# Optimization experiments

Measured on AMD Instinct MI355X. Metric: run time of the kernel, lower is better.

Reference implementation:

```python
import jax, jax.numpy as jnp
import numpy as np

N_DOC, N_WORD = 20000, 80000
N = N_DOC + N_WORD
E = 1_000_000
HID = 64
M = 10000


def setup_inputs() -> dict:
    key = jax.random.key(0)
    ks = jax.random.split(key, 10)
    doc_features = jax.random.normal(ks[0], (N_DOC, 768), dtype=jnp.float32)
    word_features = jax.random.normal(ks[1], (N_WORD, 300), dtype=jnp.float32)
    edge_index = jax.random.randint(ks[2], (2, E), 0, N, dtype=jnp.int64)
    edge_weight = jax.random.uniform(ks[3], (E,), dtype=jnp.float32)
    mask_idx = jax.random.randint(ks[4], (M,), 0, N, dtype=jnp.int64)
    y = jax.random.randint(ks[5], (N,), 0, 4, dtype=jnp.int64)
    s = 0.02
    W_lin = jax.random.normal(ks[6], (300, 768), dtype=jnp.float32) * s
    b_lin = jnp.zeros((768,), dtype=jnp.float32)
    W1 = jax.random.normal(ks[7], (768, HID), dtype=jnp.float32) * s
    b1 = jnp.zeros((HID,), dtype=jnp.float32)
    W2 = jax.random.normal(ks[8], (HID, HID), dtype=jnp.float32) * s
    b2 = jnp.zeros((HID,), dtype=jnp.float32)
    return {"doc_features": doc_features, "word_features": word_features,
            "edge_weight": edge_weight, "W_lin": W_lin, "b_lin": b_lin,
            "W1": W1, "b1": b1, "W2": W2, "b2": b2,
            "edge_index": edge_index, "mask_idx": mask_idx, "y": y}


def _gcn_norm(edge_index, edge_weight, num_nodes):
    # PyG gcn_norm: add self loops (weight 1), symmetric normalization.
    row, col = edge_index[0], edge_index[1]
    loop = jnp.arange(num_nodes, dtype=row.dtype)
    row = jnp.concatenate([row, loop])
    col = jnp.concatenate([col, loop])
    w = jnp.concatenate([edge_weight, jnp.ones((num_nodes,), edge_weight.dtype)])
    deg = jax.ops.segment_sum(w, col, num_segments=num_nodes)
    dis = jnp.where(deg > 0, jax.lax.rsqrt(jnp.maximum(deg, 1e-12)), 0.0)
    norm = dis[row] * w * dis[col]
    return row, col, norm


def _gcn_layer(x, W, b, row, col, norm, num_nodes):
    xw = x @ W                              # [N, out]
    msg = xw[row] * norm[:, None]           # gather + weight  [E+N, out]
    out = jax.ops.segment_sum(msg, col, num_segments=num_nodes)  # scatter-add
    return out + b


def reference(doc_features, word_features, edge_weight, W_lin, b_lin,
              W1, b1, W2, b2, edge_index, mask_idx, y):
    word = word_features @ W_lin + b_lin            # [N_WORD, 768]
    x = jnp.concatenate([doc_features, word], axis=0)  # [N, 768]
    num_nodes = x.shape[0]
    row, col, norm = _gcn_norm(edge_index, edge_weight, num_nodes)
    x = _gcn_layer(x, W1, b1, row, col, norm, num_nodes)
    x = jax.nn.relu(x)
    # dropout is identity in eval mode
    x = _gcn_layer(x, W2, b2, row, col, norm, num_nodes)
    return x[mask_idx], y[mask_idx]
```

## Files before the change

kernel.cpp:

```cpp
#include <hip/hip_runtime.h>


typedef __attribute__((ext_vector_type(8))) short short8;
typedef __attribute__((ext_vector_type(4))) float float4v;

__device__ __forceinline__ unsigned short f2bf(float f) {
  unsigned u = __float_as_uint(f);
  return (unsigned short)((u + 0x7FFFu + ((u >> 16) & 1u)) >> 16);
}
__device__ __forceinline__ float bf2f(unsigned short u) {
  return __uint_as_float((unsigned)u << 16);
}
__device__ __forceinline__ int permcol(int p) {
  return ((p & 3) << 4) | (p >> 2);
}

template <bool PERM>
__device__ __forceinline__ void pack_w_body(const float* __restrict__ W, int K,
                                            int nk0, unsigned short* __restrict__ pack,
                                            int tid) {
  int lane = tid & 63;
  int rest = tid >> 6;
  int k0 = rest % nk0;
  int g = rest / nk0;
  int quad = lane >> 4;
  int n = (lane & 15) + g * 16;
  short8 v;
#pragma unroll
  for (int j = 0; j < 8; ++j) {
    int k = k0 * 32 + quad * 8 + j;
    int ks = PERM ? permcol(k) : k;
    float w = (k < K) ? W[(size_t)ks * 64 + n] : 0.f;
    v[j] = (short)f2bf(w);
  }
  *(short8*)(pack + (((size_t)(g * nk0 + k0) * 64 + lane) << 3)) = v;
}

template <bool LAST, bool BF16PERM, int NK0, int CHUNK>
__device__ __forceinline__ void mfma_gemm_body(
    const float* __restrict__ X, int ldx, const float* __restrict__ lastRow,
    const unsigned short* __restrict__ Wpack,
    int K, const float* __restrict__ bias,
    void* __restrict__ outv, int R, int waveIdx) {
  int r0 = waveIdx * 16;
  if (r0 >= R) return;
  const int lane = threadIdx.x & 63;
  const int quad = lane >> 4;
  const int m = lane & 15;
  const float* xrow = nullptr;
  {
    int row = r0 + m;
    if (row < R) xrow = (LAST && row == R - 1) ? lastRow : X + (size_t)row * ldx;
  }

  float4v acc[4];
#pragma unroll
  for (int g = 0; g < 4; ++g) acc[g] = (float4v){0.f, 0.f, 0.f, 0.f};

#pragma unroll
  for (int c0 = 0; c0 < NK0; c0 += CHUNK) {
    float a[CHUNK][8];
#pragma unroll
    for (int cc = 0; cc < CHUNK; ++cc) {
      int kb = (c0 + cc) * 32 + quad * 8;
      if (xrow && kb + 8 <= K) {
        float4 v0 = *(const float4*)(xrow + kb);
        float4 v1 = *(const float4*)(xrow + kb + 4);
        a[cc][0] = v0.x; a[cc][1] = v0.y; a[cc][2] = v0.z; a[cc][3] = v0.w;
        a[cc][4] = v1.x; a[cc][5] = v1.y; a[cc][6] = v1.z; a[cc][7] = v1.w;
      } else {
#pragma unroll
        for (int j = 0; j < 8; ++j) {
          int k = kb + j;
          a[cc][j] = (xrow && k < K) ? xrow[k] : 0.f;
        }
      }
    }
#pragma unroll
    for (int cc = 0; cc < CHUNK; ++cc) {
      int k0 = c0 + cc;
      short8 bf[4];
#pragma unroll
      for (int g = 0; g < 4; ++g)
        bf[g] = *(const short8*)(Wpack + (((size_t)(g * NK0 + k0) * 64 + lane) << 3));
      short8 af;
#pragma unroll
      for (int j = 0; j < 8; ++j) af[j] = (short)f2bf(a[cc][j]);
#pragma unroll
      for (int g = 0; g < 4; ++g)
        acc[g] = __builtin_amdgcn_mfma_f32_16x16x32_bf16(af, bf[g], acc[g], 0, 0, 0);
    }
  }

  if (BF16PERM) {
    float b0 = bias ? bias[m] : 0.f;
    float b1 = bias ? bias[16 + m] : 0.f;
    float b2 = bias ? bias[32 + m] : 0.f;
    float b3 = bias ? bias[48 + m] : 0.f;
#pragma unroll
    for (int j = 0; j < 4; ++j) {
      int r = r0 + quad * 4 + j;
      if (r < R) {
        ushort4 pk;
        pk.x = f2bf(acc[0][j] + b0);
        pk.y = f2bf(acc[1][j] + b1);
        pk.z = f2bf(acc[2][j] + b2);
        pk.w = f2bf(acc[3][j] + b3);
        *(ushort4*)((unsigned short*)outv + ((size_t)r * 64 + m * 4)) = pk;
      }
    }
  } else {
#pragma unroll
    for (int g = 0; g < 4; ++g) {
      float b = bias ? bias[g * 16 + m] : 0.f;
#pragma unroll
      for (int reg = 0; reg < 4; ++reg) {
        int r = r0 + quad * 4 + reg;
        if (r < R) ((float*)outv)[(size_t)r * 64 + g * 16 + m] = acc[g][reg] + b;
      }
    }
  }
}

__global__ __launch_bounds__(256) void k_pack(
    const float* __restrict__ W1, unsigned short* __restrict__ packW1,
    const float* __restrict__ W2, unsigned short* __restrict__ packW2,
    int* __restrict__ bucketTot, int nbuck) {
  int b = blockIdx.x;
  int t = threadIdx.x;
  if (b < 24) { pack_w_body<false>(W1, 768, 24, packW1, b * 256 + t); return; }
  b -= 24;
  if (b < 2) { pack_w_body<true>(W2, 64, 2, packW2, b * 256 + t); return; }
  for (int i = t; i < nbuck + 2; i += 256) bucketTot[i] = 0;
}

__global__ __launch_bounds__(256) void k_pre(
    const float* __restrict__ Wlin, const float* __restrict__ blin,
    const unsigned short* __restrict__ packW1, float* __restrict__ WfuseB,
    int histBlocks, int fuseBlocks,
    const int* __restrict__ ei, int E, int* __restrict__ bucketTot, int nbuck,
    const float* __restrict__ doc, unsigned short* __restrict__ xw1, int ND) {
  int b = blockIdx.x;
  int t = threadIdx.x;
  if (b < histBlocks) {
    __shared__ int h[512];
    h[t] = 0; h[t + 256] = 0;
    __syncthreads();
    int e0 = b * 4096;
#pragma unroll 4
    for (int i = 0; i < 16; ++i) {
      int e = e0 + t + i * 256;
      if (e < E) atomicAdd(&h[ei[E + e] >> 8], 1);
    }
    __syncthreads();
    if (t < nbuck && h[t]) atomicAdd(bucketTot + t, h[t]);
    if (t + 256 < nbuck && h[t + 256]) atomicAdd(bucketTot + t + 256, h[t + 256]);
    return;
  }
  b -= histBlocks;
  if (b < fuseBlocks) {
    mfma_gemm_body<true, false, 24, 8>(Wlin, 768, blin, packW1, 768,
                                       nullptr, WfuseB, 301, b * 4 + (t >> 6));
    return;
  }
  b -= fuseBlocks;
  mfma_gemm_body<false, true, 24, 8>(doc, 768, nullptr, packW1, 768,
                                     nullptr, xw1, ND, b * 4 + (t >> 6));
}

__global__ __launch_bounds__(512) void k_scanB(
    const int* __restrict__ bucketTot, int nbuck,
    int* __restrict__ bucketBase, int* __restrict__ bucketRun,
    const float* __restrict__ WfuseB, unsigned short* __restrict__ packWf) {
  int t = threadIdx.x;
  if (blockIdx.x > 0) {
    pack_w_body<false>(WfuseB, 300, 10, packWf, ((int)blockIdx.x - 1) * 512 + t);
    return;
  }
  __shared__ int s[512];
  int v = (t < nbuck) ? bucketTot[t] : 0;
  s[t] = v; __syncthreads();
  for (int off = 1; off < 512; off <<= 1) {
    int x = (t >= off) ? s[t - off] : 0;
    __syncthreads();
    s[t] += x;
    __syncthreads();
  }
  if (t < nbuck) {
    int ex = s[t] - v;
    bucketBase[t] = ex;
    bucketRun[t] = ex;
  }
  if (t == nbuck - 1) bucketBase[nbuck] = s[t];
}

__global__ __launch_bounds__(256) void k_sd(
    const int* __restrict__ ei, const float* __restrict__ ew, int E,
    int scatBlocks, int* __restrict__ bucketRun, int2* __restrict__ ebuf,
    const float* __restrict__ wordf, const unsigned short* __restrict__ packWf,
    const float* __restrict__ bfuse, unsigned short* __restrict__ xw1word, int NWsd) {
  int b = blockIdx.x;
  int t = threadIdx.x;
  if (b >= scatBlocks) {
    mfma_gemm_body<false, true, 10, 5>(wordf, 300, nullptr, packWf, 300,
                                       bfuse, xw1word, NWsd, (b - scatBlocks) * 4 + (t >> 6));
    return;
  }
  __shared__ int h[512];
  __shared__ int base[512];
  __shared__ int cur[512];
  h[t] = 0; h[t + 256] = 0;
  __syncthreads();
  int e0 = b * 4096;
#pragma unroll 4
  for (int i = 0; i < 16; ++i) {
    int e = e0 + t + i * 256;
    if (e < E) atomicAdd(&h[ei[E + e] >> 8], 1);
  }
  __syncthreads();
#pragma unroll
  for (int k = t; k < 512; k += 256) {
    if (h[k]) base[k] = atomicAdd(bucketRun + k, h[k]);
    cur[k] = 0;
  }
  __syncthreads();
#pragma unroll 4
  for (int i = 0; i < 16; ++i) {
    int e = e0 + t + i * 256;
    if (e < E) {
      int d = ei[E + e];
      int bk = d >> 8;
      int r = base[bk] + atomicAdd(&cur[bk], 1);
      ebuf[r] = make_int2(ei[e] | ((d & 255) << 17), __float_as_int(ew[e]));
    }
  }
}

__global__ __launch_bounds__(256) void k_bw(
    const int2* __restrict__ ebuf, const int* __restrict__ bucketBase,
    int nbuck, int N, int* __restrict__ offs, float* __restrict__ dis,
    int2* __restrict__ entries,
    const float* __restrict__ wordf2, const unsigned short* __restrict__ packWf,
    const float* __restrict__ bfuse, unsigned short* __restrict__ xw1word2, int NW2) {
  int b = blockIdx.x;
  int t = threadIdx.x;
  if (b >= nbuck) {
    mfma_gemm_body<false, true, 10, 5>(wordf2, 300, nullptr, packWf, 300,
                                       bfuse, xw1word2, NW2, (b - nbuck) * 4 + (t >> 6));
    return;
  }
  __shared__ int scnt[256];
  __shared__ float swd[256];
  __shared__ int sscan[256];
  __shared__ int scur[256];
  int node0 = b << 8;
  int nn = min(256, N - node0);
  int estart = bucketBase[b], eend = bucketBase[b + 1];
  scnt[t] = (t < nn) ? 1 : 0;
  swd[t] = (t < nn) ? 1.f : 0.f;
  __syncthreads();
  for (int p = estart + t; p < eend; p += 256) {
    int2 e = ebuf[p];
    int low = (e.x >> 17) & 255;
    atomicAdd(&scnt[low], 1);
    atomicAdd(&swd[low], __int_as_float(e.y));
  }
  __syncthreads();
  int v = scnt[t];
  sscan[t] = v; __syncthreads();
  for (int off = 1; off < 256; off <<= 1) {
    int x = (t >= off) ? sscan[t - off] : 0;
    __syncthreads();
    sscan[t] += x;
    __syncthreads();
  }
  int excl = sscan[t] - v;
  int entriesBase = estart + node0;
  if (t < nn) {
    offs[node0 + t] = entriesBase + excl;
    dis[node0 + t] = rsqrtf(fmaxf(swd[t], 1e-12f));
    entries[entriesBase + excl] = make_int2(node0 + t, __float_as_int(1.0f));
  }
  scur[t] = excl + 1;
  if (t == 0 && b == nbuck - 1) offs[N] = entriesBase + (eend - estart) + nn;
  __syncthreads();
  for (int p = estart + t; p < eend; p += 256) {
    int2 e = ebuf[p];
    int low = (e.x >> 17) & 255;
    int r = atomicAdd(&scur[low], 1);
    entries[entriesBase + r] = make_int2(e.x & 0x1FFFF, e.y);
  }
}

__device__ __forceinline__ void row_gather2(const unsigned short* __restrict__ xin,
                                            const int2* __restrict__ entries,
                                            const float* __restrict__ dis,
                                            int p, int pe, int l32,
                                            float& ra0, float& ra1) {
  float a0 = 0.f, a1 = 0.f;
  for (; p + 8 <= pe; p += 8) {
    int2 e[8];
#pragma unroll
    for (int j = 0; j < 8; ++j) e[j] = entries[p + j];
    unsigned x[8];
    float ds[8];
#pragma unroll
    for (int j = 0; j < 8; ++j) {
      x[j] = *(const unsigned*)(xin + ((size_t)e[j].x << 6) + (l32 << 1));
      ds[j] = dis[e[j].x];
    }
#pragma unroll
    for (int j = 0; j < 8; ++j) {
      float w = __int_as_float(e[j].y) * ds[j];
      a0 = fmaf(bf2f((unsigned short)(x[j] & 0xffffu)), w, a0);
      a1 = fmaf(bf2f((unsigned short)(x[j] >> 16)), w, a1);
    }
  }
  if (p + 4 <= pe) {
    int2 e[4];
#pragma unroll
    for (int j = 0; j < 4; ++j) e[j] = entries[p + j];
    unsigned x[4];
    float ds[4];
#pragma unroll
    for (int j = 0; j < 4; ++j) {
      x[j] = *(const unsigned*)(xin + ((size_t)e[j].x << 6) + (l32 << 1));
      ds[j] = dis[e[j].x];
    }
#pragma unroll
    for (int j = 0; j < 4; ++j) {
      float w = __int_as_float(e[j].y) * ds[j];
      a0 = fmaf(bf2f((unsigned short)(x[j] & 0xffffu)), w, a0);
      a1 = fmaf(bf2f((unsigned short)(x[j] >> 16)), w, a1);
    }
    p += 4;
  }
  for (; p < pe; ++p) {
    int2 e = entries[p];
    unsigned x = *(const unsigned*)(xin + ((size_t)e.x << 6) + (l32 << 1));
    float w = __int_as_float(e.y) * dis[e.x];
    a0 = fmaf(bf2f((unsigned short)(x & 0xffffu)), w, a0);
    a1 = fmaf(bf2f((unsigned short)(x >> 16)), w, a1);
  }
  ra0 = a0; ra1 = a1;
}

__global__ void k_agg(const unsigned short* __restrict__ xin, const int2* __restrict__ entries,
                      const int* __restrict__ offs, const float* __restrict__ dis,
                      const float* __restrict__ bias, unsigned short* __restrict__ xout, int N) {
  const int tid = threadIdx.x;
  const int l32 = tid & 31;
  int i = blockIdx.x * 8 + (tid >> 5);
  if (i >= N) return;
  float a0, a1;
  row_gather2(xin, entries, dis, offs[i], offs[i + 1], l32, a0, a1);
  float d = dis[i];
  a0 = fmaxf(fmaf(a0, d, bias[permcol(2 * l32)]), 0.f);
  a1 = fmaxf(fmaf(a1, d, bias[permcol(2 * l32 + 1)]), 0.f);
  ushort2 pk;
  pk.x = f2bf(a0);
  pk.y = f2bf(a1);
  *(ushort2*)(xout + ((size_t)i << 6) + (l32 << 1)) = pk;
}

__global__ void k_agg2m(const unsigned short* __restrict__ xin, const int2* __restrict__ entries,
                        const int* __restrict__ offs, const float* __restrict__ dis,
                        const int* __restrict__ mask, const int* __restrict__ y,
                        float* __restrict__ tout, float* __restrict__ outY, int M) {
  const int tid = threadIdx.x;
  const int l32 = tid & 31;
  int o = blockIdx.x * 8 + (tid >> 5);
  if (o >= M) return;
  int i = mask[o];
  float a0, a1;
  row_gather2(xin, entries, dis, offs[i], offs[i + 1], l32, a0, a1);
  float d = dis[i];
  float2 pk;
  pk.x = a0 * d;
  pk.y = a1 * d;
  *(float2*)(tout + ((size_t)o << 6) + (l32 << 1)) = pk;
  if (l32 == 0) outY[o] = (float)y[i];
}

__global__ __launch_bounds__(256) void k_mfma_final(
    const float* __restrict__ X, const unsigned short* __restrict__ packW2,
    const float* __restrict__ b2, float* __restrict__ out, int M) {
  mfma_gemm_body<false, false, 2, 2>(X, 64, nullptr, packW2, 64,
                                     b2, out, M, blockIdx.x * 4 + (threadIdx.x >> 6));
}

extern "C" void kernel_launch(void* const* d_in, const int* in_sizes, int n_in,
                              void* d_out, int out_size, void* d_ws, size_t ws_size,
                              hipStream_t stream) {
  const float* doc   = (const float*)d_in[0];
  const float* wordf = (const float*)d_in[1];
  const float* ew    = (const float*)d_in[2];
  const float* Wlin  = (const float*)d_in[3];
  const float* blin  = (const float*)d_in[4];
  const float* W1    = (const float*)d_in[5];
  const float* b1    = (const float*)d_in[6];
  const float* W2    = (const float*)d_in[7];
  const float* b2    = (const float*)d_in[8];
  const int*   ei    = (const int*)d_in[9];
  const int*   mask  = (const int*)d_in[10];
  const int*   y     = (const int*)d_in[11];

  const int E  = in_sizes[2];
  const int M  = in_sizes[10];
  const int ND = in_sizes[0] / 768;
  const int NW = in_sizes[1] / 300;
  const int N  = ND + NW;
  const int NE = N + E;
  const int nbuck = (N + 255) >> 8;

  char* p = (char*)d_ws;
  auto carve = [&](size_t bytes) -> void* {
    void* q = (void*)p;
    p += (bytes + 255) & ~(size_t)255;
    return q;
  };
  float*          WfuseB = (float*)carve(301 * 64 * 4);
  unsigned short* packW1 = (unsigned short*)carve((size_t)4 * 24 * 64 * 8 * 2);
  unsigned short* packW2 = (unsigned short*)carve((size_t)4 * 2 * 64 * 8 * 2);
  unsigned short* packWf = (unsigned short*)carve((size_t)4 * 10 * 64 * 8 * 2);
  float* dis       = (float*)carve((size_t)N * 4);
  int*   offs      = (int*)carve(((size_t)N + 1) * 4);
  int*   bucketTot = (int*)carve((size_t)(nbuck + 2) * 4);
  int*   bucketBase= (int*)carve((size_t)(nbuck + 2) * 4);
  int*   bucketRun = (int*)carve((size_t)(nbuck + 2) * 4);
  int2*  ebuf      = (int2*)carve((size_t)E * 8);
  int2*  entries   = (int2*)carve((size_t)NE * 8);
  unsigned short* xw1 = (unsigned short*)carve((size_t)N * 64 * 2);
  unsigned short* h1  = (unsigned short*)carve((size_t)N * 64 * 2);
  float* tmask = (float*)carve((size_t)M * 64 * 4);

  k_pack<<<27, 256, 0, stream>>>(W1, packW1, W2, packW2, bucketTot, nbuck);

  const int fuseBlocks = (301 + 63) / 64;
  const int docBlocks  = (ND + 63) / 64;
  const int histBlocks = (E + 4095) / 4096;
  k_pre<<<histBlocks + fuseBlocks + docBlocks, 256, 0, stream>>>(
      Wlin, blin, packW1, WfuseB, histBlocks, fuseBlocks,
      ei, E, bucketTot, nbuck, doc, xw1, ND);

  k_scanB<<<6, 512, 0, stream>>>(bucketTot, nbuck, bucketBase, bucketRun,
                                 WfuseB, packWf);

  const int wordBlocks = (NW + 63) / 64;
  const int wsdBlocks  = wordBlocks / 2;
  const int wsdRows    = wsdBlocks * 64;
  unsigned short* xw1word = xw1 + (size_t)ND * 64;
  const float*    bfuse   = WfuseB + (size_t)300 * 64;

  k_sd<<<histBlocks + wsdBlocks, 256, 0, stream>>>(
      ei, ew, E, histBlocks, bucketRun, ebuf,
      wordf, packWf, bfuse, xw1word, wsdRows);

  k_bw<<<nbuck + (wordBlocks - wsdBlocks), 256, 0, stream>>>(
      ebuf, bucketBase, nbuck, N, offs, dis, entries,
      wordf + (size_t)wsdRows * 300, packWf, bfuse,
      xw1word + (size_t)wsdRows * 64, NW - wsdRows);

  k_agg<<<(N + 7) / 8, 256, 0, stream>>>(xw1, entries, offs, dis, b1, h1, N);

  float* out0 = (float*)d_out;
  float* outY = out0 + (size_t)M * 64;
  k_agg2m<<<(M + 7) / 8, 256, 0, stream>>>(h1, entries, offs, dis, mask, y, tmask, outY, M);
  k_mfma_final<<<(M + 63) / 64, 256, 0, stream>>>(tmask, packW2, b2, out0, M);
}
```

Baseline: 317.6 us.

## Drop scan kernel and fuse final masked aggregation with output GEMM

Removes the separate bucket-scan/weight-pack kernel. The fused Wlin·W1 GEMM now writes its result directly in packed bf16 layout plus a bias vector, and each scatter and bucket block recomputes the bucket prefix scan locally in shared memory. It also merges the masked second-layer aggregation with the final W2 MFMA GEMM into one kernel, so the intermediate tmask buffer is never written. This cuts two kernel launches and one global round trip. The cost is a redundant prefix scan in every histogram and bucket block, and a final kernel where only one wave of four runs the MFMA.

```diff
diff --git a/kernel.cpp b/kernel.cpp
--- a/kernel.cpp
+++ b/kernel.cpp
@@ -36,12 +36,12 @@
   *(short8*)(pack + (((size_t)(g * nk0 + k0) * 64 + lane) << 3)) = v;
 }
 
-template <bool LAST, bool BF16PERM, int NK0, int CHUNK>
+template <bool LAST, bool BF16PERM, bool FUSEOUT, int NK0, int CHUNK>
 __device__ __forceinline__ void mfma_gemm_body(
     const float* __restrict__ X, int ldx, const float* __restrict__ lastRow,
     const unsigned short* __restrict__ Wpack,
     int K, const float* __restrict__ bias,
-    void* __restrict__ outv, int R, int waveIdx) {
+    void* __restrict__ outv, int R, int waveIdx, float* __restrict__ bfuseOut) {
   int r0 = waveIdx * 16;
   if (r0 >= R) return;
   const int lane = threadIdx.x & 63;
@@ -92,7 +92,23 @@
     }
   }
 
-  if (BF16PERM) {
+  if (FUSEOUT) {
+    unsigned short* pf = (unsigned short*)outv;
+#pragma unroll
+    for (int g = 0; g < 4; ++g) {
+#pragma unroll
+      for (int reg = 0; reg < 4; ++reg) {
+        int r = r0 + quad * 4 + reg;
+        if (r < 300) {
+          size_t idx = ((((size_t)(g * 10 + (r >> 5))) * 64 + (((r >> 3) & 3) << 4) + m) << 3)
+                       + (r & 7);
+          pf[idx] = f2bf(acc[g][reg]);
+        } else if (r == 300) {
+          bfuseOut[g * 16 + m] = acc[g][reg];
+        }
+      }
+    }
+  } else if (BF16PERM) {
     float b0 = bias ? bias[m] : 0.f;
     float b1 = bias ? bias[16 + m] : 0.f;
     float b2 = bias ? bias[32 + m] : 0.f;
@@ -125,18 +141,22 @@
 __global__ __launch_bounds__(256) void k_pack(
     const float* __restrict__ W1, unsigned short* __restrict__ packW1,
     const float* __restrict__ W2, unsigned short* __restrict__ packW2,
-    int* __restrict__ bucketTot, int nbuck) {
+    int* __restrict__ bucketTot, int* __restrict__ runInc, int nbuck,
+    unsigned short* __restrict__ packWf) {
   int b = blockIdx.x;
   int t = threadIdx.x;
   if (b < 24) { pack_w_body<false>(W1, 768, 24, packW1, b * 256 + t); return; }
   b -= 24;
   if (b < 2) { pack_w_body<true>(W2, 64, 2, packW2, b * 256 + t); return; }
-  for (int i = t; i < nbuck + 2; i += 256) bucketTot[i] = 0;
+  for (int i = t; i < nbuck + 2; i += 256) { bucketTot[i] = 0; runInc[i] = 0; }
+  int g = t >> 6, lane = t & 63;
+  *(short8*)(packWf + (((size_t)(g * 10 + 9) * 64 + lane) << 3)) = (short8){0,0,0,0,0,0,0,0};
 }
 
 __global__ __launch_bounds__(256) void k_pre(
     const float* __restrict__ Wlin, const float* __restrict__ blin,
-    const unsigned short* __restrict__ packW1, float* __restrict__ WfuseB,
+    const unsigned short* __restrict__ packW1,
+    unsigned short* __restrict__ packWf, float* __restrict__ bfuse,
     int histBlocks, int fuseBlocks,
     const int* __restrict__ ei, int E, int* __restrict__ bucketTot, int nbuck,
     const float* __restrict__ doc, unsigned short* __restrict__ xw1, int ND) {
@@ -159,56 +179,54 @@
   }
   b -= histBlocks;
   if (b < fuseBlocks) {
-    mfma_gemm_body<true, false, 24, 8>(Wlin, 768, blin, packW1, 768,
-                                       nullptr, WfuseB, 301, b * 4 + (t >> 6));
+    mfma_gemm_body<true, false, true, 24, 8>(Wlin, 768, blin, packW1, 768,
+                                             nullptr, packWf, 301, b * 4 + (t >> 6), bfuse);
     return;
   }
   b -= fuseBlocks;
-  mfma_gemm_body<false, true, 24, 8>(doc, 768, nullptr, packW1, 768,
-                                     nullptr, xw1, ND, b * 4 + (t >> 6));
-}
-
-__global__ __launch_bounds__(512) void k_scanB(
-    const int* __restrict__ bucketTot, int nbuck,
-    int* __restrict__ bucketBase, int* __restrict__ bucketRun,
-    const float* __restrict__ WfuseB, unsigned short* __restrict__ packWf) {
-  int t = threadIdx.x;
-  if (blockIdx.x > 0) {
-    pack_w_body<false>(WfuseB, 300, 10, packWf, ((int)blockIdx.x - 1) * 512 + t);
-    return;
-  }
-  __shared__ int s[512];
-  int v = (t < nbuck) ? bucketTot[t] : 0;
-  s[t] = v; __syncthreads();
-  for (int off = 1; off < 512; off <<= 1) {
-    int x = (t >= off) ? s[t - off] : 0;
+  mfma_gemm_body<false, true, false, 24, 8>(doc, 768, nullptr, packW1, 768,
+                                            nullptr, xw1, ND, b * 4 + (t >> 6), nullptr);
+}
+
+__device__ __forceinline__ void bucket_scan(const int* __restrict__ bucketTot, int nbuck,
+                                            int* __restrict__ sc, int* __restrict__ bb,
+                                            int t) {
+  int a0 = (2 * t < nbuck) ? bucketTot[2 * t] : 0;
+  int a1 = (2 * t + 1 < nbuck) ? bucketTot[2 * t + 1] : 0;
+  sc[t] = a0 + a1;
+  __syncthreads();
+  for (int off = 1; off < 256; off <<= 1) {
+    int x = (t >= off) ? sc[t - off] : 0;
     __syncthreads();
-    s[t] += x;
+    sc[t] += x;
     __syncthreads();
   }
-  if (t < nbuck) {
-    int ex = s[t] - v;
-    bucketBase[t] = ex;
-    bucketRun[t] = ex;
-  }
-  if (t == nbuck - 1) bucketBase[nbuck] = s[t];
+  int pe = sc[t] - a0 - a1;
+  bb[2 * t] = pe;
+  bb[2 * t + 1] = pe + a0;
+  if (t == 255) bb[512] = sc[255];
+  __syncthreads();
 }
 
 __global__ __launch_bounds__(256) void k_sd(
     const int* __restrict__ ei, const float* __restrict__ ew, int E,
-    int scatBlocks, int* __restrict__ bucketRun, int2* __restrict__ ebuf,
+    int scatBlocks, const int* __restrict__ bucketTot, int nbuck,
+    int* __restrict__ runInc, int2* __restrict__ ebuf,
     const float* __restrict__ wordf, const unsigned short* __restrict__ packWf,
     const float* __restrict__ bfuse, unsigned short* __restrict__ xw1word, int NWsd) {
   int b = blockIdx.x;
   int t = threadIdx.x;
   if (b >= scatBlocks) {
-    mfma_gemm_body<false, true, 10, 5>(wordf, 300, nullptr, packWf, 300,
-                                       bfuse, xw1word, NWsd, (b - scatBlocks) * 4 + (t >> 6));
+    mfma_gemm_body<false, true, false, 10, 5>(wordf, 300, nullptr, packWf, 300,
+                                              bfuse, xw1word, NWsd,
+                                              (b - scatBlocks) * 4 + (t >> 6), nullptr);
     return;
   }
   __shared__ int h[512];
   __shared__ int base[512];
   __shared__ int cur[512];
+  __shared__ int bb[513];
+  __shared__ int sc[256];
   h[t] = 0; h[t + 256] = 0;
   __syncthreads();
   int e0 = b * 4096;
@@ -218,9 +236,10 @@
     if (e < E) atomicAdd(&h[ei[E + e] >> 8], 1);
   }
   __syncthreads();
+  bucket_scan(bucketTot, nbuck, sc, bb, t);
 #pragma unroll
   for (int k = t; k < 512; k += 256) {
-    if (h[k]) base[k] = atomicAdd(bucketRun + k, h[k]);
+    if (h[k]) base[k] = bb[k] + atomicAdd(runInc + k, h[k]);
     cur[k] = 0;
   }
   __syncthreads();
@@ -237,7 +256,7 @@
 }
 
 __global__ __launch_bounds__(256) void k_bw(
-    const int2* __restrict__ ebuf, const int* __restrict__ bucketBase,
+    const int2* __restrict__ ebuf, const int* __restrict__ bucketTot,
     int nbuck, int N, int* __restrict__ offs, float* __restrict__ dis,
     int2* __restrict__ entries,
     const float* __restrict__ wordf2, const unsigned short* __restrict__ packWf,
@@ -245,17 +264,21 @@
   int b = blockIdx.x;
   int t = threadIdx.x;
   if (b >= nbuck) {
-    mfma_gemm_body<false, true, 10, 5>(wordf2, 300, nullptr, packWf, 300,
-                                       bfuse, xw1word2, NW2, (b - nbuck) * 4 + (t >> 6));
+    mfma_gemm_body<false, true, false, 10, 5>(wordf2, 300, nullptr, packWf, 300,
+                                              bfuse, xw1word2, NW2,
+                                              (b - nbuck) * 4 + (t >> 6), nullptr);
     return;
   }
   __shared__ int scnt[256];
   __shared__ float swd[256];
   __shared__ int sscan[256];
   __shared__ int scur[256];
+  __shared__ int bb[513];
+  __shared__ int sc[256];
+  bucket_scan(bucketTot, nbuck, sc, bb, t);
+  int estart = bb[b], eend = bb[b + 1];
   int node0 = b << 8;
   int nn = min(256, N - node0);
-  int estart = bucketBase[b], eend = bucketBase[b + 1];
   scnt[t] = (t < nn) ? 1 : 0;
   swd[t] = (t < nn) ? 1.f : 0.f;
   __syncthreads();
@@ -363,30 +386,59 @@
   *(ushort2*)(xout + ((size_t)i << 6) + (l32 << 1)) = pk;
 }
 
-__global__ void k_agg2m(const unsigned short* __restrict__ xin, const int2* __restrict__ entries,
-                        const int* __restrict__ offs, const float* __restrict__ dis,
-                        const int* __restrict__ mask, const int* __restrict__ y,
-                        float* __restrict__ tout, float* __restrict__ outY, int M) {
-  const int tid = threadIdx.x;
-  const int l32 = tid & 31;
-  int o = blockIdx.x * 8 + (tid >> 5);
-  if (o >= M) return;
-  int i = mask[o];
-  float a0, a1;
-  row_gather2(xin, entries, dis, offs[i], offs[i + 1], l32, a0, a1);
-  float d = dis[i];
-  float2 pk;
-  pk.x = a0 * d;
-  pk.y = a1 * d;
-  *(float2*)(tout + ((size_t)o << 6) + (l32 << 1)) = pk;
-  if (l32 == 0) outY[o] = (float)y[i];
-}
-
-__global__ __launch_bounds__(256) void k_mfma_final(
-    const float* __restrict__ X, const unsigned short* __restrict__ packW2,
-    const float* __restrict__ b2, float* __restrict__ out, int M) {
-  mfma_gemm_body<false, false, 2, 2>(X, 64, nullptr, packW2, 64,
-                                     b2, out, M, blockIdx.x * 4 + (threadIdx.x >> 6));
+__global__ __launch_bounds__(256) void k_out(
+    const unsigned short* __restrict__ h1, const int2* __restrict__ entries,
+    const int* __restrict__ offs, const float* __restrict__ dis,
+    const int* __restrict__ mask, const int* __restrict__ y,
+    const unsigned short* __restrict__ packW2, const float* __restrict__ b2,
+    float* __restrict__ out0, float* __restrict__ outY, int M) {
+  __shared__ float rows[16][65];
+  const int t = threadIdx.x;
+  const int l32 = t & 31;
+  const int hw = t >> 5;
+  const int ob = blockIdx.x * 16;
+#pragma unroll
+  for (int rd = 0; rd < 2; ++rd) {
+    int r = rd * 8 + hw;
+    int o = ob + r;
+    float a0 = 0.f, a1 = 0.f;
+    if (o < M) {
+      int i = mask[o];
+      row_gather2(h1, entries, dis, offs[i], offs[i + 1], l32, a0, a1);
+      float d = dis[i];
+      a0 *= d; a1 *= d;
+      if (l32 == 0) outY[o] = (float)y[i];
+    }
+    rows[r][2 * l32] = a0;
+    rows[r][2 * l32 + 1] = a1;
+  }
+  __syncthreads();
+  if (t < 64) {
+    const int lane = t, quad = lane >> 4, m = lane & 15;
+    float4v acc[4];
+#pragma unroll
+    for (int g = 0; g < 4; ++g) acc[g] = (float4v){0.f, 0.f, 0.f, 0.f};
+#pragma unroll
+    for (int k0 = 0; k0 < 2; ++k0) {
+      short8 af;
+#pragma unroll
+      for (int j = 0; j < 8; ++j) af[j] = (short)f2bf(rows[m][k0 * 32 + quad * 8 + j]);
+#pragma unroll
+      for (int g = 0; g < 4; ++g) {
+        short8 bf = *(const short8*)(packW2 + (((size_t)(g * 2 + k0) * 64 + lane) << 3));
+        acc[g] = __builtin_amdgcn_mfma_f32_16x16x32_bf16(af, bf, acc[g], 0, 0, 0);
+      }
+    }
+#pragma unroll
+    for (int g = 0; g < 4; ++g) {
+      float b = b2[g * 16 + m];
+#pragma unroll
+      for (int reg = 0; reg < 4; ++reg) {
+        int r = quad * 4 + reg;
+        if (ob + r < M) out0[(size_t)(ob + r) * 64 + g * 16 + m] = acc[g][reg] + b;
+      }
+    }
+  }
 }
 
 extern "C" void kernel_launch(void* const* d_in, const int* in_sizes, int n_in,
@@ -419,45 +471,39 @@
     p += (bytes + 255) & ~(size_t)255;
     return q;
   };
-  float*          WfuseB = (float*)carve(301 * 64 * 4);
   unsigned short* packW1 = (unsigned short*)carve((size_t)4 * 24 * 64 * 8 * 2);
   unsigned short* packW2 = (unsigned short*)carve((size_t)4 * 2 * 64 * 8 * 2);
   unsigned short* packWf = (unsigned short*)carve((size_t)4 * 10 * 64 * 8 * 2);
+  float* bfuse     = (float*)carve(64 * 4);
   float* dis       = (float*)carve((size_t)N * 4);
   int*   offs      = (int*)carve(((size_t)N + 1) * 4);
   int*   bucketTot = (int*)carve((size_t)(nbuck + 2) * 4);
-  int*   bucketBase= (int*)carve((size_t)(nbuck + 2) * 4);
-  int*   bucketRun = (int*)carve((size_t)(nbuck + 2) * 4);
+  int*   runInc    = (int*)carve((size_t)(nbuck + 2) * 4);
   int2*  ebuf      = (int2*)carve((size_t)E * 8);
   int2*  entries   = (int2*)carve((size_t)NE * 8);
   unsigned short* xw1 = (unsigned short*)carve((size_t)N * 64 * 2);
   unsigned short* h1  = (unsigned short*)carve((size_t)N * 64 * 2);
-  float* tmask = (float*)carve((size_t)M * 64 * 4);
-
-  k_pack<<<27, 256, 0, stream>>>(W1, packW1, W2, packW2, bucketTot, nbuck);
+
+  k_pack<<<27, 256, 0, stream>>>(W1, packW1, W2, packW2, bucketTot, runInc, nbuck, packWf);
 
   const int fuseBlocks = (301 + 63) / 64;
   const int docBlocks  = (ND + 63) / 64;
   const int histBlocks = (E + 4095) / 4096;
   k_pre<<<histBlocks + fuseBlocks + docBlocks, 256, 0, stream>>>(
-      Wlin, blin, packW1, WfuseB, histBlocks, fuseBlocks,
+      Wlin, blin, packW1, packWf, bfuse, histBlocks, fuseBlocks,
       ei, E, bucketTot, nbuck, doc, xw1, ND);
-
-  k_scanB<<<6, 512, 0, stream>>>(bucketTot, nbuck, bucketBase, bucketRun,
-                                 WfuseB, packWf);
 
   const int wordBlocks = (NW + 63) / 64;
   const int wsdBlocks  = wordBlocks / 2;
   const int wsdRows    = wsdBlocks * 64;
   unsigned short* xw1word = xw1 + (size_t)ND * 64;
-  const float*    bfuse   = WfuseB + (size_t)300 * 64;
 
   k_sd<<<histBlocks + wsdBlocks, 256, 0, stream>>>(
-      ei, ew, E, histBlocks, bucketRun, ebuf,
+      ei, ew, E, histBlocks, bucketTot, nbuck, runInc, ebuf,
       wordf, packWf, bfuse, xw1word, wsdRows);
 
   k_bw<<<nbuck + (wordBlocks - wsdBlocks), 256, 0, stream>>>(
-      ebuf, bucketBase, nbuck, N, offs, dis, entries,
+      ebuf, bucketTot, nbuck, N, offs, dis, entries,
       wordf + (size_t)wsdRows * 300, packWf, bfuse,
       xw1word + (size_t)wsdRows * 64, NW - wsdRows);
 
@@ -465,6 +511,6 @@
 
   float* out0 = (float*)d_out;
   float* outY = out0 + (size_t)M * 64;
-  k_agg2m<<<(M + 7) / 8, 256, 0, stream>>>(h1, entries, offs, dis, mask, y, tmask, outY, M);
-  k_mfma_final<<<(M + 63) / 64, 256, 0, stream>>>(tmask, packW2, b2, out0, M);
-}
+  k_out<<<(M + 15) / 16, 256, 0, stream>>>(
+      h1, entries, offs, dis, mask, y, packW2, b2, out0, outY, M);
+}
```

New measurement: 318.4 us. About the same (+0.2%).
